# Performance work log

Hardware: AMD Instinct MI355X
Metric: run time of the kernel (lower is better)

The kernel has to match this reference:

```python
import jax, jax.numpy as jnp
import numpy as np

N_NODES = 100000
D_SRC = 128
D_DST = 128
D_OUT = 256
N_EDGES = 600000


def setup_inputs() -> dict:
    key = jax.random.key(0)
    k1, k2, k3, k4, k5 = jax.random.split(key, 5)
    x_src = jax.random.normal(k1, (N_NODES, D_SRC), dtype=jnp.float32)
    x_dst = jax.random.normal(k2, (N_NODES, D_DST), dtype=jnp.float32)
    edge_index = jax.random.randint(k3, (2, N_EDGES), 0, N_NODES, dtype=jnp.int64)
    # Linear(in_src + in_dst, out): torch stores W as [out, in]
    fan_in = D_SRC + D_DST
    bound = 1.0 / np.sqrt(fan_in)
    W = jax.random.uniform(k4, (D_OUT, fan_in), minval=-bound, maxval=bound, dtype=jnp.float32)
    b = jax.random.uniform(k5, (D_OUT,), minval=-bound, maxval=bound, dtype=jnp.float32)
    return {"x_src": x_src, "x_dst": x_dst, "edge_index": edge_index, "W": W, "b": b}


def reference(x_src, x_dst, edge_index, W, b):
    src_idx, dst_idx = edge_index[0], edge_index[1]
    n_dst = x_dst.shape[0]
    x_j = x_src[src_idx]                                  # [E, D_SRC] gather
    summed = jax.ops.segment_sum(x_j, dst_idx, num_segments=n_dst)   # [N, D_SRC]
    count = jax.ops.segment_sum(jnp.ones((src_idx.shape[0],), dtype=x_src.dtype),
                                dst_idx, num_segments=n_dst)          # [N]
    agg = summed / jnp.maximum(count, 1.0)[:, None]        # scatter-mean
    h = jnp.concatenate([x_dst, agg], axis=-1)             # [N, D_DST+D_SRC]
    return jax.nn.relu(h @ W.T + b)                        # [N, D_OUT]
```

## Files before the change

### kernel.cpp

```cpp
#include <hip/hip_runtime.h>

#define N_NODES 100000
#define D_SRC 128
#define D_OUT 256
#define K_DIM 256
#define CAP 32
#define OVF_CAP 2048

typedef __attribute__((ext_vector_type(8))) short short8;
typedef __attribute__((ext_vector_type(4))) float float4v;
typedef __attribute__((ext_vector_type(4))) unsigned int uint4v;

__device__ inline unsigned short f2bf(float f) {
    unsigned int u = __float_as_uint(f);
    u += 0x7FFF + ((u >> 16) & 1);
    return (unsigned short)(u >> 16);
}
__device__ inline float bf_lo(unsigned int u) { return __uint_as_float(u << 16); }
__device__ inline float bf_hi(unsigned int u) { return __uint_as_float(u & 0xFFFF0000u); }

#define PREP_SRC_BLOCKS 12500
#define PREP_DST_BLOCKS 6250
#define PREP_W_BLOCKS   32
#define PREP_Z_BLOCKS   98
#define PREP_BLOCKS (PREP_SRC_BLOCKS + PREP_DST_BLOCKS + PREP_W_BLOCKS + PREP_Z_BLOCKS)

__global__ __launch_bounds__(256) void prep_kernel(
    const float* __restrict__ x_src,
    const float* __restrict__ x_dst,
    const float* __restrict__ W,
    unsigned short* __restrict__ xsb,
    unsigned short* __restrict__ xdsw,
    unsigned short* __restrict__ wsw,
    int* __restrict__ deg)
{
    int b = blockIdx.x;
    if (b < PREP_SRC_BLOCKS) {
        int i = b * 256 + threadIdx.x;
        float4 v = ((const float4*)x_src)[i];
        ushort4 o;
        o.x = f2bf(v.x); o.y = f2bf(v.y); o.z = f2bf(v.z); o.w = f2bf(v.w);
        ((ushort4*)xsb)[i] = o;
    } else if (b < PREP_SRC_BLOCKS + PREP_DST_BLOCKS) {
        int t = (b - PREP_SRC_BLOCKS) * 256 + threadIdx.x;
        int r = t >> 4;
        int g = t & 15;
        const float4* p = (const float4*)(x_dst + (size_t)r * 128 + g * 8);
        float4 v0 = p[0], v1 = p[1];
        union { unsigned short s[8]; short8 v; } pk;
        pk.s[0] = f2bf(v0.x); pk.s[1] = f2bf(v0.y);
        pk.s[2] = f2bf(v0.z); pk.s[3] = f2bf(v0.w);
        pk.s[4] = f2bf(v1.x); pk.s[5] = f2bf(v1.y);
        pk.s[6] = f2bf(v1.z); pk.s[7] = f2bf(v1.w);
        size_t gr = ((size_t)(r >> 4) * 4 + (g >> 2)) * 64 + (r & 15) + ((g & 3) << 4);
        ((short8*)xdsw)[gr] = pk.v;
    } else if (b < PREP_SRC_BLOCKS + PREP_DST_BLOCKS + PREP_W_BLOCKS) {
        int t = (b - PREP_SRC_BLOCKS - PREP_DST_BLOCKS) * 256 + threadIdx.x;
        int r = t >> 5;
        int g = t & 31;
        const float4* p = (const float4*)(W + (size_t)r * 256 + g * 8);
        float4 v0 = p[0], v1 = p[1];
        union { unsigned short s[8]; short8 v; } pk;
        pk.s[0] = f2bf(v0.x); pk.s[1] = f2bf(v0.y);
        pk.s[2] = f2bf(v0.z); pk.s[3] = f2bf(v0.w);
        pk.s[4] = f2bf(v1.x); pk.s[5] = f2bf(v1.y);
        pk.s[6] = f2bf(v1.z); pk.s[7] = f2bf(v1.w);
        size_t gr = ((size_t)(r >> 4) * 8 + (g >> 2)) * 64 + (r & 15) + ((g & 3) << 4);
        ((short8*)wsw)[gr] = pk.v;
    } else {
        int i = (b - PREP_SRC_BLOCKS - PREP_DST_BLOCKS - PREP_W_BLOCKS) * 256 + threadIdx.x;
        if (i < (N_NODES + 4) / 4)
            ((int4*)deg)[i] = make_int4(0, 0, 0, 0);
    }
}

__global__ __launch_bounds__(256) void bucket_kernel(
    const int* __restrict__ ei,
    int* __restrict__ deg,
    int* __restrict__ ovf_cnt,
    int* __restrict__ ovf,
    int* __restrict__ bucket,
    int n_edges)
{
    int t = blockIdx.x * 256 + threadIdx.x;
    int e0 = 2 * t;
    if (e0 + 1 < n_edges) {
        int2 s2 = ((const int2*)ei)[t];
        int2 d2 = ((const int2*)(ei + n_edges))[t];
        int pos0 = atomicAdd(deg + d2.x, 1);
        if (pos0 < CAP) {
            bucket[(size_t)d2.x * CAP + pos0] = s2.x;
        } else {
            int o = atomicAdd(ovf_cnt, 1);
            if (o < OVF_CAP) { ovf[2 * o] = s2.x; ovf[2 * o + 1] = d2.x; }
        }
        int pos1 = atomicAdd(deg + d2.y, 1);
        if (pos1 < CAP) {
            bucket[(size_t)d2.y * CAP + pos1] = s2.y;
        } else {
            int o = atomicAdd(ovf_cnt, 1);
            if (o < OVF_CAP) { ovf[2 * o] = s2.y; ovf[2 * o + 1] = d2.y; }
        }
    } else if (e0 < n_edges) {
        int s = ei[e0];
        int d = ei[n_edges + e0];
        int pos = atomicAdd(deg + d, 1);
        if (pos < CAP) {
            bucket[(size_t)d * CAP + pos] = s;
        } else {
            int o = atomicAdd(ovf_cnt, 1);
            if (o < OVF_CAP) { ovf[2 * o] = s; ovf[2 * o + 1] = d; }
        }
    }
}

#define G_ISSUE8(U, V, B, I0, I1, I2, I3, N0, N1, N2, N3)                     \
    {                                                                         \
        int r_ = (B) + grp;                                                   \
        { bool v_ = r_ < N0; V[0] = v_; int s_ = __shfl(I0, r_);              \
          s_ = v_ ? s_ : 0;                                                   \
          U[0] = *(const uint4v*)(xsb + (size_t)s_ * D_SRC + gcol * 8); }     \
        { bool v_ = r_ < N1; V[1] = v_; int s_ = __shfl(I1, r_);              \
          s_ = v_ ? s_ : 0;                                                   \
          U[1] = *(const uint4v*)(xsb + (size_t)s_ * D_SRC + gcol * 8); }     \
        { bool v_ = r_ < N2; V[2] = v_; int s_ = __shfl(I2, r_);              \
          s_ = v_ ? s_ : 0;                                                   \
          U[2] = *(const uint4v*)(xsb + (size_t)s_ * D_SRC + gcol * 8); }     \
        { bool v_ = r_ < N3; V[3] = v_; int s_ = __shfl(I3, r_);              \
          s_ = v_ ? s_ : 0;                                                   \
          U[3] = *(const uint4v*)(xsb + (size_t)s_ * D_SRC + gcol * 8); }     \
    }

#define G_ACC1(ACC, W)                                                       \
    ACC[0] += bf_lo(W[0]); ACC[1] += bf_hi(W[0]);                            \
    ACC[2] += bf_lo(W[1]); ACC[3] += bf_hi(W[1]);                            \
    ACC[4] += bf_lo(W[2]); ACC[5] += bf_hi(W[2]);                            \
    ACC[6] += bf_lo(W[3]); ACC[7] += bf_hi(W[3]);

#define G_ACCUM8(U, V, A0, A1, A2, A3)                                       \
    if (V[0]) { G_ACC1(A0, U[0]) }                                           \
    if (V[1]) { G_ACC1(A1, U[1]) }                                           \
    if (V[2]) { G_ACC1(A2, U[2]) }                                           \
    if (V[3]) { G_ACC1(A3, U[3]) }

__global__ __launch_bounds__(256) void gather_kernel(
    const unsigned short* __restrict__ xsb,
    const int*   __restrict__ deg,
    const int*   __restrict__ bucket,
    const int*   __restrict__ ovf_cnt,
    const int*   __restrict__ ovf,
    unsigned int* __restrict__ aggsw)
{
    int wid  = threadIdx.x >> 6;
    int lane = threadIdx.x & 63;
    int wbase = (blockIdx.x * 4 + wid) * 8;
    int grp  = lane >> 4;
    int gcol = lane & 15;

    int dl = deg[wbase + (lane & 7)];
    int dtA0 = __shfl(dl, 0), dtA1 = __shfl(dl, 1);
    int dtA2 = __shfl(dl, 2), dtA3 = __shfl(dl, 3);
    int dtB0 = __shfl(dl, 4), dtB1 = __shfl(dl, 5);
    int dtB2 = __shfl(dl, 6), dtB3 = __shfl(dl, 7);
    int nA0 = min(dtA0, CAP), nA1 = min(dtA1, CAP);
    int nA2 = min(dtA2, CAP), nA3 = min(dtA3, CAP);
    int nB0 = min(dtB0, CAP), nB1 = min(dtB1, CAP);
    int nB2 = min(dtB2, CAP), nB3 = min(dtB3, CAP);

    int iA0 = bucket[(size_t)(wbase + 0) * CAP + (lane & 31)];
    int iA1 = bucket[(size_t)(wbase + 1) * CAP + (lane & 31)];
    int iA2 = bucket[(size_t)(wbase + 2) * CAP + (lane & 31)];
    int iA3 = bucket[(size_t)(wbase + 3) * CAP + (lane & 31)];
    int iB0 = bucket[(size_t)(wbase + 4) * CAP + (lane & 31)];
    int iB1 = bucket[(size_t)(wbase + 5) * CAP + (lane & 31)];
    int iB2 = bucket[(size_t)(wbase + 6) * CAP + (lane & 31)];
    int iB3 = bucket[(size_t)(wbase + 7) * CAP + (lane & 31)];

    float accA0[8] = {0,0,0,0,0,0,0,0}, accA1[8] = {0,0,0,0,0,0,0,0};
    float accA2[8] = {0,0,0,0,0,0,0,0}, accA3[8] = {0,0,0,0,0,0,0,0};
    float accB0[8] = {0,0,0,0,0,0,0,0}, accB1[8] = {0,0,0,0,0,0,0,0};
    float accB2[8] = {0,0,0,0,0,0,0,0}, accB3[8] = {0,0,0,0,0,0,0,0};

    int maxn = max(max(max(nA0, nA1), max(nA2, nA3)),
                   max(max(nB0, nB1), max(nB2, nB3)));

    uint4v uAa[4], uAb[4], uBa[4], uBb[4];
    bool   vAa[4], vAb[4], vBa[4], vBb[4];
    if (maxn > 0) {
        G_ISSUE8(uAa, vAa, 0, iA0, iA1, iA2, iA3, nA0, nA1, nA2, nA3)
        G_ISSUE8(uBa, vBa, 0, iB0, iB1, iB2, iB3, nB0, nB1, nB2, nB3)
        int bb = 0;
        while (true) {
            if (bb + 4 < maxn) {
                G_ISSUE8(uAb, vAb, bb + 4, iA0, iA1, iA2, iA3, nA0, nA1, nA2, nA3)
                G_ISSUE8(uBb, vBb, bb + 4, iB0, iB1, iB2, iB3, nB0, nB1, nB2, nB3)
            }
            G_ACCUM8(uAa, vAa, accA0, accA1, accA2, accA3)
            G_ACCUM8(uBa, vBa, accB0, accB1, accB2, accB3)
            bb += 4;
            if (bb >= maxn) break;
            if (bb + 4 < maxn) {
                G_ISSUE8(uAa, vAa, bb + 4, iA0, iA1, iA2, iA3, nA0, nA1, nA2, nA3)
                G_ISSUE8(uBa, vBa, bb + 4, iB0, iB1, iB2, iB3, nB0, nB1, nB2, nB3)
            }
            G_ACCUM8(uAb, vAb, accA0, accA1, accA2, accA3)
            G_ACCUM8(uBb, vBb, accB0, accB1, accB2, accB3)
            bb += 4;
            if (bb >= maxn) break;
        }
    }

    if ((dtA0 > CAP) | (dtA1 > CAP) | (dtA2 > CAP) | (dtA3 > CAP) |
        (dtB0 > CAP) | (dtB1 > CAP) | (dtB2 > CAP) | (dtB3 > CAP)) {
        int oc = *ovf_cnt;
        if (oc > OVF_CAP) oc = OVF_CAP;
        for (int o = 0; o < oc; ++o) {
            int od  = ovf[2 * o + 1];
            int rel = od - wbase;
            if (rel >= 0 && rel < 8) {
                int s0 = ovf[2 * o];
                uint4v w = *(const uint4v*)(xsb + (size_t)s0 * D_SRC + gcol * 8);
                if (grp == 0) {
                    if      (rel == 0) { G_ACC1(accA0, w) }
                    else if (rel == 1) { G_ACC1(accA1, w) }
                    else if (rel == 2) { G_ACC1(accA2, w) }
                    else if (rel == 3) { G_ACC1(accA3, w) }
                    else if (rel == 4) { G_ACC1(accB0, w) }
                    else if (rel == 5) { G_ACC1(accB1, w) }
                    else if (rel == 6) { G_ACC1(accB2, w) }
                    else               { G_ACC1(accB3, w) }
                }
            }
        }
    }

    #pragma unroll
    for (int k = 0; k < 8; ++k) {
        accA0[k] += __shfl_xor(accA0[k], 16); accA0[k] += __shfl_xor(accA0[k], 32);
        accA1[k] += __shfl_xor(accA1[k], 16); accA1[k] += __shfl_xor(accA1[k], 32);
        accA2[k] += __shfl_xor(accA2[k], 16); accA2[k] += __shfl_xor(accA2[k], 32);
        accA3[k] += __shfl_xor(accA3[k], 16); accA3[k] += __shfl_xor(accA3[k], 32);
        accB0[k] += __shfl_xor(accB0[k], 16); accB0[k] += __shfl_xor(accB0[k], 32);
        accB1[k] += __shfl_xor(accB1[k], 16); accB1[k] += __shfl_xor(accB1[k], 32);
        accB2[k] += __shfl_xor(accB2[k], 16); accB2[k] += __shfl_xor(accB2[k], 32);
        accB3[k] += __shfl_xor(accB3[k], 16); accB3[k] += __shfl_xor(accB3[k], 32);
    }

    {
        int dsel = dtA0;
        dsel = (grp == 1) ? dtA1 : dsel;
        dsel = (grp == 2) ? dtA2 : dsel;
        dsel = (grp == 3) ? dtA3 : dsel;
        float inv = 1.0f / (float)((dsel > 1) ? dsel : 1);
        float sum[8];
        #pragma unroll
        for (int k = 0; k < 8; ++k) {
            float v = accA0[k];
            v = (grp == 1) ? accA1[k] : v;
            v = (grp == 2) ? accA2[k] : v;
            v = (grp == 3) ? accA3[k] : v;
            sum[k] = v * inv;
        }
        uint4v o;
        o[0] = (unsigned)f2bf(sum[0]) | ((unsigned)f2bf(sum[1]) << 16);
        o[1] = (unsigned)f2bf(sum[2]) | ((unsigned)f2bf(sum[3]) << 16);
        o[2] = (unsigned)f2bf(sum[4]) | ((unsigned)f2bf(sum[5]) << 16);
        o[3] = (unsigned)f2bf(sum[6]) | ((unsigned)f2bf(sum[7]) << 16);
        int node = wbase + grp;
        size_t gr = ((size_t)(node >> 4) * 4 + (gcol >> 2)) * 64
                  + (node & 15) + ((gcol & 3) << 4);
        ((uint4v*)aggsw)[gr] = o;
    }
    {
        int dsel = dtB0;
        dsel = (grp == 1) ? dtB1 : dsel;
        dsel = (grp == 2) ? dtB2 : dsel;
        dsel = (grp == 3) ? dtB3 : dsel;
        float inv = 1.0f / (float)((dsel > 1) ? dsel : 1);
        float sum[8];
        #pragma unroll
        for (int k = 0; k < 8; ++k) {
            float v = accB0[k];
            v = (grp == 1) ? accB1[k] : v;
            v = (grp == 2) ? accB2[k] : v;
            v = (grp == 3) ? accB3[k] : v;
            sum[k] = v * inv;
        }
        uint4v o;
        o[0] = (unsigned)f2bf(sum[0]) | ((unsigned)f2bf(sum[1]) << 16);
        o[1] = (unsigned)f2bf(sum[2]) | ((unsigned)f2bf(sum[3]) << 16);
        o[2] = (unsigned)f2bf(sum[4]) | ((unsigned)f2bf(sum[5]) << 16);
        o[3] = (unsigned)f2bf(sum[6]) | ((unsigned)f2bf(sum[7]) << 16);
        int node = wbase + 4 + grp;
        size_t gr = ((size_t)(node >> 4) * 4 + (gcol >> 2)) * 64
                  + (node & 15) + ((gcol & 3) << 4);
        ((uint4v*)aggsw)[gr] = o;
    }
}

__global__ __launch_bounds__(256) void mfma_gemm_kernel(
    const short8* __restrict__ xdsw,
    const short8* __restrict__ aggsw,
    const short8* __restrict__ wsw,
    const float* __restrict__ bias,
    float*       __restrict__ out)
{
    __shared__ float eps[4][16][68];

    int wave = threadIdx.x >> 6;
    int lane = threadIdx.x & 63;
    int lrow = lane & 15;
    int kq   = lane >> 4;
    int mb   = blockIdx.x;
    int m0   = mb * 64;
    int n0   = wave * 64;

    bool mok[4];
    #pragma unroll
    for (int mf = 0; mf < 4; ++mf) mok[mf] = (m0 + mf * 16) < N_NODES;

    const short8* Ax = xdsw  + (size_t)mb * 1024 + lane;
    const short8* Ag = aggsw + (size_t)mb * 1024 + lane;
    const short8* Bw = wsw   + (size_t)wave * 2048 + lane;

    float4v acc[4][4];
    #pragma unroll
    for (int i = 0; i < 4; ++i)
        #pragma unroll
        for (int j = 0; j < 4; ++j)
            acc[i][j] = (float4v){0.f, 0.f, 0.f, 0.f};

    const short8 zfrag = (short8){0,0,0,0,0,0,0,0};
    short8 a[2][4], b[2][4];

    #pragma unroll
    for (int mf = 0; mf < 4; ++mf)
        a[0][mf] = mok[mf] ? Ax[mf * 256] : zfrag;
    #pragma unroll
    for (int nf = 0; nf < 4; ++nf)
        b[0][nf] = Bw[nf * 512];

    #pragma unroll
    for (int kc = 0; kc < 8; ++kc) {
        const int cur = kc & 1, nxt = cur ^ 1;
        if (kc < 7) {
            const int k1 = kc + 1;
            const short8* A = (k1 < 4) ? Ax : Ag;
            const int kk = (k1 < 4) ? k1 : (k1 - 4);
            #pragma unroll
            for (int mf = 0; mf < 4; ++mf)
                a[nxt][mf] = mok[mf] ? A[mf * 256 + kk * 64] : zfrag;
            #pragma unroll
            for (int nf = 0; nf < 4; ++nf)
                b[nxt][nf] = Bw[nf * 512 + k1 * 64];
        }
        #pragma unroll
        for (int mf = 0; mf < 4; ++mf)
            #pragma unroll
            for (int nf = 0; nf < 4; ++nf)
                acc[mf][nf] = __builtin_amdgcn_mfma_f32_16x16x32_bf16(
                    a[cur][mf], b[cur][nf], acc[mf][nf], 0, 0, 0);
    }

    float bv[4];
    #pragma unroll
    for (int nf = 0; nf < 4; ++nf)
        bv[nf] = bias[n0 + nf * 16 + lrow];

    int srow   = lane >> 4;
    int schunk = lane & 15;

    #pragma unroll
    for (int mf = 0; mf < 4; ++mf) {
        if (!mok[mf]) continue;
        #pragma unroll
        for (int nf = 0; nf < 4; ++nf)
            #pragma unroll
            for (int r = 0; r < 4; ++r)
                eps[wave][kq * 4 + r][nf * 16 + lrow] =
                    fmaxf(acc[mf][nf][r] + bv[nf], 0.f);
        asm volatile("s_waitcnt lgkmcnt(0)" ::: "memory");
        #pragma unroll
        for (int c = 0; c < 4; ++c) {
            int row  = c * 4 + srow;
            float4v v = *(const float4v*)&eps[wave][row][schunk * 4];
            int grow = m0 + mf * 16 + row;
            __builtin_nontemporal_store(v,
                (float4v*)(out + (size_t)grow * D_OUT + n0 + schunk * 4));
        }
        asm volatile("s_waitcnt lgkmcnt(0)" ::: "memory");
    }
}

extern "C" void kernel_launch(void* const* d_in, const int* in_sizes, int n_in,
                              void* d_out, int out_size, void* d_ws, size_t ws_size,
                              hipStream_t stream) {
    const float* x_src = (const float*)d_in[0];
    const float* x_dst = (const float*)d_in[1];
    const int*   ei    = (const int*)d_in[2];
    const float* W     = (const float*)d_in[3];
    const float* bias  = (const float*)d_in[4];
    float* out = (float*)d_out;

    int n_edges = in_sizes[2] / 2;

    int* deg     = (int*)d_ws;
    int* ovf_cnt = deg + N_NODES;
    int* ovf     = ovf_cnt + 4;
    unsigned short* wsw   = (unsigned short*)(ovf + OVF_CAP * 2);
    unsigned short* aggsw = wsw + (size_t)D_OUT * K_DIM;
    unsigned short* xdsw  = aggsw + (size_t)(N_NODES / 16) * 4 * 64 * 8;

    int* bucket = (int*)d_out;
    unsigned short* xsb = (unsigned short*)(bucket + (size_t)N_NODES * CAP);

    prep_kernel<<<PREP_BLOCKS, 256, 0, stream>>>(
        x_src, x_dst, W, xsb, xdsw, wsw, deg);

    int n_pairs = (n_edges + 1) / 2;
    bucket_kernel<<<(n_pairs + 255) / 256, 256, 0, stream>>>(
        ei, deg, ovf_cnt, ovf, bucket, n_edges);

    gather_kernel<<<(N_NODES + 31) / 32, 256, 0, stream>>>(
        xsb, deg, bucket, ovf_cnt, ovf, (unsigned int*)aggsw);

    mfma_gemm_kernel<<<(N_NODES + 63) / 64, 256, 0, stream>>>(
        (const short8*)xdsw, (const short8*)aggsw, (const short8*)wsw, bias, out);
}
```

Baseline: 286.2 us.

## Fuse edge bucketing into prep kernel and zero degree counters with memset

The separate bucket kernel is folded into the prep kernel as its first block range, so edge bucketing runs alongside the bf16 conversion of x_src, x_dst and W. Zeroing of deg and ovf_cnt moves from prep blocks to a hipMemsetAsync ahead of the launch. This removes one kernel launch and the serialization between prep and bucketing, letting atomic scatter traffic overlap with streaming conversion. Bucket blocks now handle one edge per thread instead of two, and the memset adds a small extra stream operation.

```diff
diff --git a/kernel.cpp b/kernel.cpp
--- a/kernel.cpp
+++ b/kernel.cpp
@@ -22,19 +22,38 @@
 #define PREP_SRC_BLOCKS 12500
 #define PREP_DST_BLOCKS 6250
 #define PREP_W_BLOCKS   32
-#define PREP_Z_BLOCKS   98
-#define PREP_BLOCKS (PREP_SRC_BLOCKS + PREP_DST_BLOCKS + PREP_W_BLOCKS + PREP_Z_BLOCKS)
 
 __global__ __launch_bounds__(256) void prep_kernel(
     const float* __restrict__ x_src,
     const float* __restrict__ x_dst,
     const float* __restrict__ W,
+    const int*   __restrict__ ei,
     unsigned short* __restrict__ xsb,
     unsigned short* __restrict__ xdsw,
     unsigned short* __restrict__ wsw,
-    int* __restrict__ deg)
+    int* __restrict__ deg,
+    int* __restrict__ ovf_cnt,
+    int* __restrict__ ovf,
+    int* __restrict__ bucket,
+    int n_edges, int nb_bucket)
 {
     int b = blockIdx.x;
+    if (b < nb_bucket) {
+        int e = b * 256 + threadIdx.x;
+        if (e < n_edges) {
+            int s = ei[e];
+            int d = ei[n_edges + e];
+            int pos = atomicAdd(deg + d, 1);
+            if (pos < CAP) {
+                bucket[(size_t)d * CAP + pos] = s;
+            } else {
+                int o = atomicAdd(ovf_cnt, 1);
+                if (o < OVF_CAP) { ovf[2 * o] = s; ovf[2 * o + 1] = d; }
+            }
+        }
+        return;
+    }
+    b -= nb_bucket;
     if (b < PREP_SRC_BLOCKS) {
         int i = b * 256 + threadIdx.x;
         float4 v = ((const float4*)x_src)[i];
@@ -54,7 +73,7 @@
         pk.s[6] = f2bf(v1.z); pk.s[7] = f2bf(v1.w);
         size_t gr = ((size_t)(r >> 4) * 4 + (g >> 2)) * 64 + (r & 15) + ((g & 3) << 4);
         ((short8*)xdsw)[gr] = pk.v;
-    } else if (b < PREP_SRC_BLOCKS + PREP_DST_BLOCKS + PREP_W_BLOCKS) {
+    } else {
         int t = (b - PREP_SRC_BLOCKS - PREP_DST_BLOCKS) * 256 + threadIdx.x;
         int r = t >> 5;
         int g = t & 31;
@@ -67,50 +86,6 @@
         pk.s[6] = f2bf(v1.z); pk.s[7] = f2bf(v1.w);
         size_t gr = ((size_t)(r >> 4) * 8 + (g >> 2)) * 64 + (r & 15) + ((g & 3) << 4);
         ((short8*)wsw)[gr] = pk.v;
-    } else {
-        int i = (b - PREP_SRC_BLOCKS - PREP_DST_BLOCKS - PREP_W_BLOCKS) * 256 + threadIdx.x;
-        if (i < (N_NODES + 4) / 4)
-            ((int4*)deg)[i] = make_int4(0, 0, 0, 0);
-    }
-}
-
-__global__ __launch_bounds__(256) void bucket_kernel(
-    const int* __restrict__ ei,
-    int* __restrict__ deg,
-    int* __restrict__ ovf_cnt,
-    int* __restrict__ ovf,
-    int* __restrict__ bucket,
-    int n_edges)
-{
-    int t = blockIdx.x * 256 + threadIdx.x;
-    int e0 = 2 * t;
-    if (e0 + 1 < n_edges) {
-        int2 s2 = ((const int2*)ei)[t];
-        int2 d2 = ((const int2*)(ei + n_edges))[t];
-        int pos0 = atomicAdd(deg + d2.x, 1);
-        if (pos0 < CAP) {
-            bucket[(size_t)d2.x * CAP + pos0] = s2.x;
-        } else {
-            int o = atomicAdd(ovf_cnt, 1);
-            if (o < OVF_CAP) { ovf[2 * o] = s2.x; ovf[2 * o + 1] = d2.x; }
-        }
-        int pos1 = atomicAdd(deg + d2.y, 1);
-        if (pos1 < CAP) {
-            bucket[(size_t)d2.y * CAP + pos1] = s2.y;
-        } else {
-            int o = atomicAdd(ovf_cnt, 1);
-            if (o < OVF_CAP) { ovf[2 * o] = s2.y; ovf[2 * o + 1] = d2.y; }
-        }
-    } else if (e0 < n_edges) {
-        int s = ei[e0];
-        int d = ei[n_edges + e0];
-        int pos = atomicAdd(deg + d, 1);
-        if (pos < CAP) {
-            bucket[(size_t)d * CAP + pos] = s;
-        } else {
-            int o = atomicAdd(ovf_cnt, 1);
-            if (o < OVF_CAP) { ovf[2 * o] = s; ovf[2 * o + 1] = d; }
-        }
     }
 }
 
@@ -414,12 +389,13 @@
     int* bucket = (int*)d_out;
     unsigned short* xsb = (unsigned short*)(bucket + (size_t)N_NODES * CAP);
 
-    prep_kernel<<<PREP_BLOCKS, 256, 0, stream>>>(
-        x_src, x_dst, W, xsb, xdsw, wsw, deg);
-
-    int n_pairs = (n_edges + 1) / 2;
-    bucket_kernel<<<(n_pairs + 255) / 256, 256, 0, stream>>>(
-        ei, deg, ovf_cnt, ovf, bucket, n_edges);
+    hipMemsetAsync(d_ws, 0, (N_NODES + 4) * sizeof(int), stream);
+
+    int nb_bucket = (n_edges + 255) / 256;
+    int prep_blocks = nb_bucket + PREP_SRC_BLOCKS + PREP_DST_BLOCKS + PREP_W_BLOCKS;
+    prep_kernel<<<prep_blocks, 256, 0, stream>>>(
+        x_src, x_dst, W, ei, xsb, xdsw, wsw,
+        deg, ovf_cnt, ovf, bucket, n_edges, nb_bucket);
 
     gather_kernel<<<(N_NODES + 31) / 32, 256, 0, stream>>>(
         xsb, deg, bucket, ovf_cnt, ovf, (unsigned int*)aggsw);
```

Measured after the change: 287.9 us. About the same (+0.6%).
